# Kernel tuning notes

Measured on AMD Instinct MI355X. Metric: run time of the kernel, lower is better.

The kernel has to match this reference:

```python
import jax, jax.numpy as jnp
import numpy as np

ALPHA = 0.0005
TAU = 0.2


def setup_inputs() -> dict:
    key = jax.random.key(0)
    k1, k2, k3 = jax.random.split(key, 3)
    output = jax.random.normal(k1, (8192, 1000), dtype=jnp.float32)
    target = jax.random.normal(k2, (8192, 1000), dtype=jnp.float32)
    conv_w = jax.random.normal(k3, (256, 256, 128, 3), dtype=jnp.float32)
    return {"output": output, "target": target, "conv_w": conv_w}


def reference(output, target, conv_w):
    # base loss (nn.MSELoss with default 'mean' reduction)
    loss = jnp.mean((output - target) ** 2)

    # Diversity regularizer: pairwise cosine similarity between slices
    # conv_w[:, :, i, :] along dim 2 ('filters' = size(2) in the original).
    F = conv_w.shape[2]
    # V: [F, D] with D = out_ch * in_ch * kw
    V = jnp.transpose(conv_w, (2, 0, 1, 3)).reshape(F, -1)
    norms = jnp.linalg.norm(V, axis=1)                      # [F]
    G = (V @ V.T) / (norms[:, None] * norms[None, :])       # [F, F] cosine Gram

    # keep entries with tau < sim <= 1 and i != j
    offdiag = ~jnp.eye(F, dtype=bool)
    mask = (G > TAU) & (G <= 1.0) & offdiag
    reg = jnp.sum(jnp.where(mask, G, jnp.zeros((), dtype=G.dtype)))

    return loss + ALPHA * reg
```

## Files before the change

### kernel.cpp

```cpp
#include <hip/hip_runtime.h>
#include <hip/hip_bf16.h>


typedef __attribute__((ext_vector_type(8))) short bf16x8;
typedef __attribute__((ext_vector_type(4))) float f32x4;

#define ALPHA 0.0005f
#define TAU 0.2f

#define FDIM 128
#define TSTRIDE 52
#define GRAM_NBLK 512
#define CHUNK_F4 3072
#define GRAM_ELEMS 16384
#define NPAIRQ 8192
#define MSE_N4 2048000
#define MSE_NBLK 2048

__device__ __forceinline__ unsigned int pack_bf2(float lo, float hi) {
    union { float f; unsigned int u; } a, b;
    a.f = lo; b.f = hi;
    unsigned int al = (a.u + 0x7fffu + ((a.u >> 16) & 1u)) >> 16;
    unsigned int bh = (b.u + 0x7fffu + ((b.u >> 16) & 1u)) & 0xffff0000u;
    return (al & 0xffffu) | bh;
}

__global__ void __launch_bounds__(256) mse_kernel(
        const float* __restrict__ o, const float* __restrict__ t,
        float* __restrict__ mse_part) {
    __shared__ float red[4];
    const int tid = threadIdx.x;
    const float4* o4 = reinterpret_cast<const float4*>(o);
    const float4* t4 = reinterpret_cast<const float4*>(t);
    float s = 0.f;
    for (int i = blockIdx.x * 256 + tid; i < MSE_N4; i += MSE_NBLK * 256) {
        float4 a = o4[i], b = t4[i];
        float dx = a.x - b.x, dy = a.y - b.y, dz = a.z - b.z, dw = a.w - b.w;
        s += dx * dx + dy * dy + dz * dz + dw * dw;
    }
    for (int off = 32; off; off >>= 1) s += __shfl_down(s, off);
    if ((tid & 63) == 0) red[tid >> 6] = s;
    __syncthreads();
    if (tid == 0) mse_part[blockIdx.x] = red[0] + red[1] + red[2] + red[3];
}

__device__ __forceinline__ void loadc(const f32x4* __restrict__ src4,
                                      size_t base4, f32x4 (&R)[12]) {
#pragma unroll
    for (int it = 0; it < 6; ++it) {
        R[2 * it]     = src4[base4 + 16 * it];
        R[2 * it + 1] = src4[base4 + 96 + 16 * it];
    }
    __builtin_amdgcn_sched_barrier(0);
}

__device__ __forceinline__ void convertc(const f32x4 (&R)[12],
                                         unsigned int* __restrict__ tb,
                                         int p, int q) {
#pragma unroll
    for (int it = 0; it < 6; ++it)
#pragma unroll
        for (int u = 0; u < 4; ++u) {
            const int idx = (q + 16 * it) * 4 + u;
            const int f = idx / 3;
            const int k = idx - 3 * f;
            tb[f * TSTRIDE + k * 16 + p] = pack_bf2(R[2 * it][u], R[2 * it + 1][u]);
        }
}

__device__ __forceinline__ void barrier_tile() {
    asm volatile("s_waitcnt lgkmcnt(0)" ::: "memory");
    __builtin_amdgcn_sched_barrier(0);
    __builtin_amdgcn_s_barrier();
    __builtin_amdgcn_sched_barrier(0);
}

__device__ __forceinline__ void mfmaph(const unsigned short* __restrict__ tu,
                                       int wave, int colr, int hi8,
                                       f32x4 (&acc0)[8], f32x4 (&acc1)[8]) {
#pragma unroll
    for (int ks = 0; ks < 3; ++ks) {
        const int koff = ks * 32 + hi8;
        bf16x8 a0 = *reinterpret_cast<const bf16x8*>(
            &tu[(wave * 32 + colr) * (TSTRIDE * 2) + koff]);
        bf16x8 a1 = *reinterpret_cast<const bf16x8*>(
            &tu[(wave * 32 + 16 + colr) * (TSTRIDE * 2) + koff]);
#pragma unroll
        for (int cc = 0; cc < 8; ++cc) {
            bf16x8 b = *reinterpret_cast<const bf16x8*>(
                &tu[(cc * 16 + colr) * (TSTRIDE * 2) + koff]);
            acc0[cc] = __builtin_amdgcn_mfma_f32_16x16x32_bf16(a0, b, acc0[cc], 0, 0, 0);
            acc1[cc] = __builtin_amdgcn_mfma_f32_16x16x32_bf16(a1, b, acc1[cc], 0, 0, 0);
        }
    }
}

__global__ void __launch_bounds__(256, 2) gram_kernel(
        const float* __restrict__ conv, unsigned int* __restrict__ pp) {
    __shared__ unsigned int tile[2][FDIM * TSTRIDE];
    const int tid = threadIdx.x;
    const int lane = tid & 63;
    const int wave = tid >> 6;
    const int p = tid >> 4;
    const int q = tid & 15;
    const int colr = lane & 15;
    const int hi8 = (lane >> 4) * 8;
    const unsigned short* t0u = reinterpret_cast<const unsigned short*>(tile[0]);
    const unsigned short* t1u = reinterpret_cast<const unsigned short*>(tile[1]);

    f32x4 acc0[8], acc1[8];
#pragma unroll
    for (int cc = 0; cc < 8; ++cc) { acc0[cc] = (f32x4)0.f; acc1[cc] = (f32x4)0.f; }

    const f32x4* src4 = reinterpret_cast<const f32x4*>(conv);
    const size_t cb = (size_t)blockIdx.x * (4 * CHUNK_F4) + (2 * p) * 96 + q;

    f32x4 RA[12], RB[12];
    loadc(src4, cb + 0 * CHUNK_F4, RA);

    loadc(src4, cb + 1 * CHUNK_F4, RB);
    convertc(RA, tile[0], p, q);
    barrier_tile();
    mfmaph(t0u, wave, colr, hi8, acc0, acc1);
    loadc(src4, cb + 2 * CHUNK_F4, RA);
    convertc(RB, tile[1], p, q);
    barrier_tile();
    mfmaph(t1u, wave, colr, hi8, acc0, acc1);
    loadc(src4, cb + 3 * CHUNK_F4, RB);
    convertc(RA, tile[0], p, q);
    barrier_tile();
    mfmaph(t0u, wave, colr, hi8, acc0, acc1);
    convertc(RB, tile[1], p, q);
    barrier_tile();
    mfmaph(t1u, wave, colr, hi8, acc0, acc1);

    unsigned int* myp = pp + (size_t)blockIdx.x * NPAIRQ;
    const int rsub = (lane >> 4) << 2;
#pragma unroll
    for (int cc = 0; cc < 8; ++cc) {
        const int col = cc * 16 + colr;
#pragma unroll
        for (int j = 0; j < 4; ++j) {
            const int pr = wave * 16 + rsub + j;
            myp[pr * FDIM + col] = pack_bf2(acc0[cc][j], acc1[cc][j]);
        }
    }
}

__global__ void __launch_bounds__(256) reduce_kernel(
        const unsigned int* __restrict__ pp, float* __restrict__ gram) {
    __shared__ float red[16][16][2];
    const int tid = threadIdx.x;
    const int u = tid & 15;
    const int s = tid >> 4;
    const int qq = blockIdx.x * 16 + u;
    float lo = 0.f, hi = 0.f;
#pragma unroll 8
    for (int b = s * 32; b < s * 32 + 32; ++b) {
        const unsigned int v = pp[(size_t)b * NPAIRQ + qq];
        lo += __uint_as_float(v << 16);
        hi += __uint_as_float(v & 0xffff0000u);
    }
    red[s][u][0] = lo; red[s][u][1] = hi;
    __syncthreads();
    if (tid < 32) {
        const int u2 = tid >> 1, h = tid & 1;
        float x = 0.f;
#pragma unroll
        for (int s2 = 0; s2 < 16; ++s2) x += red[s2][u2][h];
        gram[(blockIdx.x * 16 + u2) * 2 + h] = x;
    }
}

__global__ void __launch_bounds__(256) finalize_kernel(
        const float* __restrict__ gram, const float* __restrict__ mse_part,
        float* __restrict__ out) {
    __shared__ float rn[FDIM];
    __shared__ float redS[4], redM[4];
    const int tid = threadIdx.x;
    if (tid < FDIM) {
        const int row = tid;
        const int pr = (row >> 5) * 16 + (row & 15);
        const int h = (row >> 4) & 1;
        rn[row] = rsqrtf(gram[(pr * FDIM + row) * 2 + h]);
    }
    __syncthreads();
    float s = 0.f;
    for (int i = tid; i < GRAM_ELEMS; i += 256) {
        const int h = i & 1;
        const int qq = i >> 1;
        const int col = qq & 127;
        const int pr = qq >> 7;
        const int row = (pr >> 4) * 32 + (pr & 15) + (h << 4);
        const float g = gram[i] * rn[row] * rn[col];
        if (row != col && g > TAU && g <= 1.0f) s += g;
    }
    float m = 0.f;
#pragma unroll 8
    for (int j = 0; j < 8; ++j) m += mse_part[tid * 8 + j];
    for (int off = 32; off; off >>= 1) {
        s += __shfl_down(s, off);
        m += __shfl_down(m, off);
    }
    if ((tid & 63) == 0) { redS[tid >> 6] = s; redM[tid >> 6] = m; }
    __syncthreads();
    if (tid == 0)
        out[0] = (redM[0] + redM[1] + redM[2] + redM[3]) * (1.0f / 8192000.0f) +
                 ALPHA * (redS[0] + redS[1] + redS[2] + redS[3]);
}

extern "C" void kernel_launch(void* const* d_in, const int* in_sizes, int n_in,
                              void* d_out, int out_size, void* d_ws, size_t ws_size,
                              hipStream_t stream) {
    const float* output = (const float*)d_in[0];
    const float* target = (const float*)d_in[1];
    const float* conv   = (const float*)d_in[2];
    float* out = (float*)d_out;

    float* wsf       = (float*)d_ws;
    float* mse_part  = wsf;
    float* gram      = wsf + MSE_NBLK;
    unsigned int* pp = (unsigned int*)(wsf + MSE_NBLK + GRAM_ELEMS);
    (void)ws_size;

    gram_kernel<<<GRAM_NBLK, 256, 0, stream>>>(conv, pp);
    mse_kernel<<<MSE_NBLK, 256, 0, stream>>>(output, target, mse_part);
    reduce_kernel<<<NPAIRQ / 16, 256, 0, stream>>>(pp, gram);
    finalize_kernel<<<1, 256, 0, stream>>>(gram, mse_part, out);
}
```

Before: 60.88 us.

## Fuse MSE and Gram kernels; load MFMA fragments directly from global memory

Merges the MSE reduction and the Gram computation into a single 256-block kernel, so one launch covers both and the MSE loads overlap the first conv prefetch. The Gram path drops the LDS transpose tiles: each wave builds bf16 MFMA fragments straight from float3 global loads, with one zero-padded k slot, and keeps a full 128x128 accumulator (64 f32x4) in registers. The four waves' partials are summed through shared memory before a per-block write. This halves the partial buffers that reduce_kernel must sum. The costs are very high register pressure at one block per CU, a quarter of MFMA k-width spent on padding, and unaligned float3 loads.

```diff
diff --git a/kernel.cpp b/kernel.cpp
--- a/kernel.cpp
+++ b/kernel.cpp
@@ -9,13 +9,11 @@
 #define TAU 0.2f
 
 #define FDIM 128
-#define TSTRIDE 52
-#define GRAM_NBLK 512
-#define CHUNK_F4 3072
+#define NBLK 256
 #define GRAM_ELEMS 16384
 #define NPAIRQ 8192
 #define MSE_N4 2048000
-#define MSE_NBLK 2048
+#define NTILES 256
 
 __device__ __forceinline__ unsigned int pack_bf2(float lo, float hi) {
     union { float f; unsigned int u; } a, b;
@@ -25,125 +23,114 @@
     return (al & 0xffffu) | bh;
 }
 
-__global__ void __launch_bounds__(256) mse_kernel(
+__device__ __forceinline__ bf16x8 make_frag(const float3& a, const float3& b) {
+    union { bf16x8 v; unsigned int u[4]; } r;
+    r.u[0] = pack_bf2(a.x, a.y);
+    r.u[1] = pack_bf2(a.z, b.x);
+    r.u[2] = pack_bf2(b.y, b.z);
+    r.u[3] = 0;
+    return r.v;
+}
+
+__device__ __forceinline__ void load_oct(const float* __restrict__ lp,
+                                         float3 (&L)[8][2]) {
+#pragma unroll
+    for (int tt = 0; tt < 8; ++tt)
+#pragma unroll
+        for (int e = 0; e < 2; ++e)
+            L[tt][e] = *reinterpret_cast<const float3*>(lp + tt * 48 + e * 384);
+    __builtin_amdgcn_sched_barrier(0);
+}
+
+__device__ __forceinline__ void step_oct(const float3 (&L)[8][2],
+                                         f32x4 (&acc)[8][8]) {
+    bf16x8 fr[8];
+#pragma unroll
+    for (int tt = 0; tt < 8; ++tt) fr[tt] = make_frag(L[tt][0], L[tt][1]);
+#pragma unroll
+    for (int r = 0; r < 8; ++r)
+#pragma unroll
+        for (int c = 0; c < 8; ++c)
+            acc[r][c] = __builtin_amdgcn_mfma_f32_16x16x32_bf16(
+                fr[r], fr[c], acc[r][c], 0, 0, 0);
+}
+
+__global__ void __launch_bounds__(256, 1) fused_kernel(
         const float* __restrict__ o, const float* __restrict__ t,
-        float* __restrict__ mse_part) {
+        const float* __restrict__ conv,
+        float* __restrict__ mse_part, unsigned int* __restrict__ pp) {
+    __shared__ unsigned int pk[4][NPAIRQ];
     __shared__ float red[4];
-    const int tid = threadIdx.x;
-    const float4* o4 = reinterpret_cast<const float4*>(o);
-    const float4* t4 = reinterpret_cast<const float4*>(t);
-    float s = 0.f;
-    for (int i = blockIdx.x * 256 + tid; i < MSE_N4; i += MSE_NBLK * 256) {
-        float4 a = o4[i], b = t4[i];
-        float dx = a.x - b.x, dy = a.y - b.y, dz = a.z - b.z, dw = a.w - b.w;
-        s += dx * dx + dy * dy + dz * dz + dw * dw;
-    }
-    for (int off = 32; off; off >>= 1) s += __shfl_down(s, off);
-    if ((tid & 63) == 0) red[tid >> 6] = s;
-    __syncthreads();
-    if (tid == 0) mse_part[blockIdx.x] = red[0] + red[1] + red[2] + red[3];
-}
-
-__device__ __forceinline__ void loadc(const f32x4* __restrict__ src4,
-                                      size_t base4, f32x4 (&R)[12]) {
-#pragma unroll
-    for (int it = 0; it < 6; ++it) {
-        R[2 * it]     = src4[base4 + 16 * it];
-        R[2 * it + 1] = src4[base4 + 96 + 16 * it];
-    }
-    __builtin_amdgcn_sched_barrier(0);
-}
-
-__device__ __forceinline__ void convertc(const f32x4 (&R)[12],
-                                         unsigned int* __restrict__ tb,
-                                         int p, int q) {
-#pragma unroll
-    for (int it = 0; it < 6; ++it)
-#pragma unroll
-        for (int u = 0; u < 4; ++u) {
-            const int idx = (q + 16 * it) * 4 + u;
-            const int f = idx / 3;
-            const int k = idx - 3 * f;
-            tb[f * TSTRIDE + k * 16 + p] = pack_bf2(R[2 * it][u], R[2 * it + 1][u]);
-        }
-}
-
-__device__ __forceinline__ void barrier_tile() {
-    asm volatile("s_waitcnt lgkmcnt(0)" ::: "memory");
-    __builtin_amdgcn_sched_barrier(0);
-    __builtin_amdgcn_s_barrier();
-    __builtin_amdgcn_sched_barrier(0);
-}
-
-__device__ __forceinline__ void mfmaph(const unsigned short* __restrict__ tu,
-                                       int wave, int colr, int hi8,
-                                       f32x4 (&acc0)[8], f32x4 (&acc1)[8]) {
-#pragma unroll
-    for (int ks = 0; ks < 3; ++ks) {
-        const int koff = ks * 32 + hi8;
-        bf16x8 a0 = *reinterpret_cast<const bf16x8*>(
-            &tu[(wave * 32 + colr) * (TSTRIDE * 2) + koff]);
-        bf16x8 a1 = *reinterpret_cast<const bf16x8*>(
-            &tu[(wave * 32 + 16 + colr) * (TSTRIDE * 2) + koff]);
-#pragma unroll
-        for (int cc = 0; cc < 8; ++cc) {
-            bf16x8 b = *reinterpret_cast<const bf16x8*>(
-                &tu[(cc * 16 + colr) * (TSTRIDE * 2) + koff]);
-            acc0[cc] = __builtin_amdgcn_mfma_f32_16x16x32_bf16(a0, b, acc0[cc], 0, 0, 0);
-            acc1[cc] = __builtin_amdgcn_mfma_f32_16x16x32_bf16(a1, b, acc1[cc], 0, 0, 0);
-        }
-    }
-}
-
-__global__ void __launch_bounds__(256, 2) gram_kernel(
-        const float* __restrict__ conv, unsigned int* __restrict__ pp) {
-    __shared__ unsigned int tile[2][FDIM * TSTRIDE];
     const int tid = threadIdx.x;
     const int lane = tid & 63;
     const int wave = tid >> 6;
-    const int p = tid >> 4;
-    const int q = tid & 15;
-    const int colr = lane & 15;
-    const int hi8 = (lane >> 4) * 8;
-    const unsigned short* t0u = reinterpret_cast<const unsigned short*>(tile[0]);
-    const unsigned short* t1u = reinterpret_cast<const unsigned short*>(tile[1]);
-
-    f32x4 acc0[8], acc1[8];
-#pragma unroll
-    for (int cc = 0; cc < 8; ++cc) { acc0[cc] = (f32x4)0.f; acc1[cc] = (f32x4)0.f; }
-
-    const f32x4* src4 = reinterpret_cast<const f32x4*>(conv);
-    const size_t cb = (size_t)blockIdx.x * (4 * CHUNK_F4) + (2 * p) * 96 + q;
-
-    f32x4 RA[12], RB[12];
-    loadc(src4, cb + 0 * CHUNK_F4, RA);
-
-    loadc(src4, cb + 1 * CHUNK_F4, RB);
-    convertc(RA, tile[0], p, q);
-    barrier_tile();
-    mfmaph(t0u, wave, colr, hi8, acc0, acc1);
-    loadc(src4, cb + 2 * CHUNK_F4, RA);
-    convertc(RB, tile[1], p, q);
-    barrier_tile();
-    mfmaph(t1u, wave, colr, hi8, acc0, acc1);
-    loadc(src4, cb + 3 * CHUNK_F4, RB);
-    convertc(RA, tile[0], p, q);
-    barrier_tile();
-    mfmaph(t0u, wave, colr, hi8, acc0, acc1);
-    convertc(RB, tile[1], p, q);
-    barrier_tile();
-    mfmaph(t1u, wave, colr, hi8, acc0, acc1);
+    const int g = lane >> 4;
+    const int fl = lane & 15;
+
+    const int W = blockIdx.x * 4 + wave;
+    const float* lp = conv + (size_t)W * 24576 + (2 * g) * 384 + fl * 3;
+
+    float3 L0[8][2], L1[8][2];
+    load_oct(lp, L0);
+
+    {
+        const int gid = blockIdx.x * 256 + tid;
+        const f32x4* o4 = reinterpret_cast<const f32x4*>(o);
+        const f32x4* t4 = reinterpret_cast<const f32x4*>(t);
+        float s = 0.f;
+#pragma unroll 8
+        for (int p = 0; p < 31; ++p) {
+            const int i = gid + p * 65536;
+            f32x4 a = o4[i], b = t4[i];
+            f32x4 d = a - b;
+            s += d[0]*d[0] + d[1]*d[1] + d[2]*d[2] + d[3]*d[3];
+        }
+        if (gid < MSE_N4 - 31 * 65536) {
+            const int i = gid + 31 * 65536;
+            f32x4 a = o4[i], b = t4[i];
+            f32x4 d = a - b;
+            s += d[0]*d[0] + d[1]*d[1] + d[2]*d[2] + d[3]*d[3];
+        }
+        for (int off = 32; off; off >>= 1) s += __shfl_down(s, off);
+        if (lane == 0) red[wave] = s;
+        __syncthreads();
+        if (tid == 0) mse_part[blockIdx.x] = red[0] + red[1] + red[2] + red[3];
+    }
+
+    f32x4 acc[8][8];
+#pragma unroll
+    for (int r = 0; r < 8; ++r)
+#pragma unroll
+        for (int c = 0; c < 8; ++c) acc[r][c] = (f32x4)0.f;
+
+#pragma unroll
+    for (int oo = 0; oo < 8; oo += 2) {
+        load_oct(lp + (oo + 1) * 3072, L1);
+        step_oct(L0, acc);
+        if (oo + 2 < 8) load_oct(lp + (oo + 2) * 3072, L0);
+        step_oct(L1, acc);
+    }
+
+#pragma unroll
+    for (int m = 0; m < 4; ++m)
+#pragma unroll
+        for (int c = 0; c < 8; ++c)
+#pragma unroll
+            for (int j = 0; j < 4; ++j)
+                pk[wave][(m * 16 + g * 4 + j) * FDIM + c * 16 + fl] =
+                    pack_bf2(acc[2 * m][c][j], acc[2 * m + 1][c][j]);
+    __syncthreads();
 
     unsigned int* myp = pp + (size_t)blockIdx.x * NPAIRQ;
-    const int rsub = (lane >> 4) << 2;
-#pragma unroll
-    for (int cc = 0; cc < 8; ++cc) {
-        const int col = cc * 16 + colr;
-#pragma unroll
-        for (int j = 0; j < 4; ++j) {
-            const int pr = wave * 16 + rsub + j;
-            myp[pr * FDIM + col] = pack_bf2(acc0[cc][j], acc1[cc][j]);
+    for (int e = tid; e < NPAIRQ; e += 256) {
+        float lo = 0.f, hi = 0.f;
+#pragma unroll
+        for (int w = 0; w < 4; ++w) {
+            const unsigned int v = pk[w][e];
+            lo += __uint_as_float(v << 16);
+            hi += __uint_as_float(v & 0xffff0000u);
         }
+        myp[e] = pack_bf2(lo, hi);
     }
 }
 
@@ -156,7 +143,7 @@
     const int qq = blockIdx.x * 16 + u;
     float lo = 0.f, hi = 0.f;
 #pragma unroll 8
-    for (int b = s * 32; b < s * 32 + 32; ++b) {
+    for (int b = s * 16; b < s * 16 + 16; ++b) {
         const unsigned int v = pp[(size_t)b * NPAIRQ + qq];
         lo += __uint_as_float(v << 16);
         hi += __uint_as_float(v & 0xffff0000u);
@@ -195,9 +182,7 @@
         const float g = gram[i] * rn[row] * rn[col];
         if (row != col && g > TAU && g <= 1.0f) s += g;
     }
-    float m = 0.f;
-#pragma unroll 8
-    for (int j = 0; j < 8; ++j) m += mse_part[tid * 8 + j];
+    float m = mse_part[tid];
     for (int off = 32; off; off >>= 1) {
         s += __shfl_down(s, off);
         m += __shfl_down(m, off);
@@ -219,12 +204,11 @@
 
     float* wsf       = (float*)d_ws;
     float* mse_part  = wsf;
-    float* gram      = wsf + MSE_NBLK;
-    unsigned int* pp = (unsigned int*)(wsf + MSE_NBLK + GRAM_ELEMS);
+    float* gram      = wsf + 256;
+    unsigned int* pp = (unsigned int*)(wsf + 256 + GRAM_ELEMS);
     (void)ws_size;
 
-    gram_kernel<<<GRAM_NBLK, 256, 0, stream>>>(conv, pp);
-    mse_kernel<<<MSE_NBLK, 256, 0, stream>>>(output, target, mse_part);
+    fused_kernel<<<NBLK, 256, 0, stream>>>(output, target, conv, mse_part, pp);
     reduce_kernel<<<NPAIRQ / 16, 256, 0, stream>>>(pp, gram);
     finalize_kernel<<<1, 256, 0, stream>>>(gram, mse_part, out);
 }
```

Measured after the change: 57.94 us. -4.8%, faster.
